# Kernel tuning notes

Hardware: AMD Instinct MI355X
Metric: run time of the kernel (lower is better)

Reference implementation:

```python
import jax, jax.numpy as jnp
import numpy as np

N_EMBD = 1024
HIDDEN = 4 * N_EMBD          # 4096
ADAPT = HIDDEN // 16         # 256
NUM_EXPERTS = 8
B, S = 4, 2048
LN_EPS = 1e-5


def setup_inputs() -> dict:
    key = jax.random.key(0)
    ks = jax.random.split(key, 8)
    x = jax.random.normal(ks[0], (B, S, N_EMBD), dtype=jnp.float32)
    # top-1 routing: one-hot expert weights (disjoint masks, standard MoE dispatch)
    route = jax.random.randint(ks[1], (B, S), 0, NUM_EXPERTS)
    expert_weights = jax.nn.one_hot(route, NUM_EXPERTS, dtype=jnp.float32)
    up_scale = 0.1 / N_EMBD ** 0.5
    adapt_scale0 = 0.1 / HIDDEN ** 0.5
    adapt_scale = 0.01 / ADAPT ** 0.5
    W_up = jax.random.normal(ks[2], (HIDDEN, N_EMBD), dtype=jnp.float32) * up_scale
    W_adapt = jax.random.normal(ks[3], (ADAPT, HIDDEN), dtype=jnp.float32) * adapt_scale0
    W_exp_adapters = jax.random.normal(ks[4], (NUM_EXPERTS, ADAPT, ADAPT), dtype=jnp.float32) * adapt_scale
    ln_gamma = jnp.ones((NUM_EXPERTS, ADAPT), dtype=jnp.float32)
    ln_beta = jnp.zeros((NUM_EXPERTS, ADAPT), dtype=jnp.float32)
    W_expert_proj = jax.random.normal(ks[5], (HIDDEN, ADAPT), dtype=jnp.float32) * adapt_scale
    W_out = jax.random.normal(ks[6], (N_EMBD, HIDDEN), dtype=jnp.float32) * adapt_scale
    return {"x": x, "expert_weights": expert_weights, "W_up": W_up,
            "W_adapt": W_adapt, "W_exp_adapters": W_exp_adapters,
            "ln_gamma": ln_gamma, "ln_beta": ln_beta,
            "W_expert_proj": W_expert_proj, "W_out": W_out}


def reference(x, expert_weights, W_up, W_adapt, W_exp_adapters, ln_gamma, ln_beta, W_expert_proj, W_out):
    b, s, d = x.shape
    T = b * s
    E = expert_weights.shape[-1]
    xt = x.reshape(T, d)

    # shared MLP path (silu(up_proj(x))) -> output_proj
    h = jax.nn.silu(xt @ W_up.T)                      # [T, HIDDEN]
    shared_out = (h @ W_out.T).reshape(b, s, d)       # [B, S, D]

    active = expert_weights.reshape(T, E) > 0         # [T, E]
    any_active = jnp.any(active, axis=-1)             # [T]
    last_idx = E - 1 - jnp.argmax(active[:, ::-1], axis=-1)  # [T]

    # pre_adapt (silu(up) recomputed == h) -> adapt_proj
    a = h @ W_adapt.T                                 # [T, ADAPT]
    # per-expert adapter linears, then select the winning expert per token
    a_all = jnp.einsum('td,eod->teo', a, W_exp_adapters)      # [T, E, ADAPT]
    a_sel = jnp.take_along_axis(a_all, last_idx[:, None, None], axis=1)[:, 0]  # [T, ADAPT]

    # per-expert LayerNorm params gathered per token
    g = ln_gamma[last_idx]                            # [T, ADAPT]
    be = ln_beta[last_idx]
    mu = jnp.mean(a_sel, axis=-1, keepdims=True)
    var = jnp.mean(jnp.square(a_sel - mu), axis=-1, keepdims=True)
    a_norm = (a_sel - mu) * jax.lax.rsqrt(var + LN_EPS) * g + be

    h2 = a_norm @ W_expert_proj.T                     # [T, HIDDEN]
    e_out = h2 @ W_out.T                              # [T, D]
    combined = jnp.where(any_active[:, None], e_out, 0.0).reshape(b, s, d)
    return shared_out + 0.1 * combined
```

## Files before the change

### kernel.cpp

```cpp
#include <hip/hip_runtime.h>
#include <cstdint>

#define TOK  8192
#define DEMB 1024
#define HID  4096
#define ADP  256
#define NEXP 8
#define KAUG 4352

typedef __bf16 bf16x8 __attribute__((ext_vector_type(8)));
typedef float  f32x4  __attribute__((ext_vector_type(4)));

__device__ __forceinline__ unsigned short f2bf(float f) {
  unsigned int u = __float_as_uint(f);
  u += 0x7fffu + ((u >> 16) & 1u);
  return (unsigned short)(u >> 16);
}
__device__ __forceinline__ float bf2f(unsigned short b) {
  return __uint_as_float(((unsigned int)b) << 16);
}

__global__ __launch_bounds__(256) void convert_all(
    const float* __restrict__ x, const float* __restrict__ wup,
    const float* __restrict__ wout, const float* __restrict__ wadapt,
    const float* __restrict__ wexp, const float* __restrict__ ew,
    const float* __restrict__ wp,
    unsigned short* __restrict__ xb, unsigned short* __restrict__ wub,
    unsigned short* __restrict__ wob, unsigned short* __restrict__ wab,
    unsigned short* __restrict__ web, int* __restrict__ route,
    unsigned short* __restrict__ wpT) {
  __shared__ float tile[64][65];
  int b = blockIdx.x;
  if (b >= 8992) {
    int wli = b - 8992;
    const int h0 = (wli & 63) * 64;
    const int a0 = (wli >> 6) * 64;
    const int t = threadIdx.x;
    const int r = t >> 4;
    const int c = (t & 15) * 4;
#pragma unroll
    for (int p = 0; p < 4; ++p) {
      int row = p * 16 + r;
      float4 v = *(const float4*)(wp + (size_t)(h0 + row) * ADP + a0 + c);
      tile[c + 0][row] = v.x;
      tile[c + 1][row] = v.y;
      tile[c + 2][row] = v.z;
      tile[c + 3][row] = v.w;
    }
    __syncthreads();
#pragma unroll
    for (int q = 0; q < 2; ++q) {
      int idx = q * 256 + t;
      int al = idx >> 3;
      int hg = (idx & 7) * 8;
      unsigned int w0 = (unsigned int)f2bf(tile[al][hg + 0]) |
                        ((unsigned int)f2bf(tile[al][hg + 1]) << 16);
      unsigned int w1 = (unsigned int)f2bf(tile[al][hg + 2]) |
                        ((unsigned int)f2bf(tile[al][hg + 3]) << 16);
      unsigned int w2 = (unsigned int)f2bf(tile[al][hg + 4]) |
                        ((unsigned int)f2bf(tile[al][hg + 5]) << 16);
      unsigned int w3 = (unsigned int)f2bf(tile[al][hg + 6]) |
                        ((unsigned int)f2bf(tile[al][hg + 7]) << 16);
      *(uint4*)(wpT + (size_t)(a0 + al) * HID + h0 + hg) =
          make_uint4(w0, w1, w2, w3);
    }
    return;
  }
  if (b >= 8960) {
    int t = (b - 8960) * 256 + threadIdx.x;
    const float* p = ew + (size_t)t * NEXP;
    int r = -1;
#pragma unroll
    for (int e = 0; e < NEXP; ++e)
      if (p[e] > 0.f) r = e;
    route[t] = r;
    return;
  }
  const float* src; unsigned short* dst; int lb; bool strided = false;
  if      (b < 4096) { src = x;      dst = xb;  lb = b; }
  else if (b < 6144) { src = wup;    dst = wub; lb = b - 4096; }
  else if (b < 8192) { src = wout;   dst = wob; lb = b - 6144; strided = true; }
  else if (b < 8704) { src = wadapt; dst = wab; lb = b - 8192; }
  else               { src = wexp;   dst = web; lb = b - 8704; }
  size_t base = (size_t)lb * 2048;
#pragma unroll
  for (int h = 0; h < 2; ++h) {
    size_t off = base + (size_t)h * 1024 + (size_t)threadIdx.x * 4;
    float4 v = *(const float4*)(src + off);
    ushort4 o;
    o.x = f2bf(v.x); o.y = f2bf(v.y); o.z = f2bf(v.z); o.w = f2bf(v.w);
    size_t doff = strided ? (off >> 12) * KAUG + (off & 4095) : off;
    *(ushort4*)(dst + doff) = o;
  }
}

__device__ __forceinline__ void remap_xcd(int li, int gx, int gy,
                                          int& bx, int& by) {
  int xcd = li & 7;
  int slot = li >> 3;
  bx = slot % gx;
  by = xcd * (gy >> 3) + slot / gx;
}

__device__ __forceinline__ void read_frag4(const unsigned short* base, int lane,
                                           int rowoff, int kk, bf16x8* dst) {
#pragma unroll
  for (int i = 0; i < 4; ++i) {
    int rr = rowoff + i * 16 + (lane & 15);
    int sw = ((kk >> 3) + (lane >> 4)) ^ (lane & 7);
    dst[i] = *(const bf16x8*)&base[rr * 64 + sw * 8];
  }
}

template <int NH>
__device__ __forceinline__ void mfma8(const bf16x8* af, const bf16x8* bf,
                                      f32x4 acc[4][4]) {
#pragma unroll
  for (int mt = 0; mt < 4; ++mt)
#pragma unroll
    for (int q = 0; q < 2; ++q)
      acc[mt][NH * 2 + q] = __builtin_amdgcn_mfma_f32_16x16x32_bf16(
          af[mt], bf[NH * 2 + q], acc[mt][NH * 2 + q], 0, 0, 0);
}

#define PHASE_MID()                                       \
  __builtin_amdgcn_s_barrier();                           \
  asm volatile("s_waitcnt lgkmcnt(0)" ::: "memory");      \
  __builtin_amdgcn_sched_barrier(0);                      \
  __builtin_amdgcn_s_setprio(1)

#define PHASE_END()                                       \
  __builtin_amdgcn_s_setprio(0);                          \
  __builtin_amdgcn_sched_barrier(0);                      \
  __builtin_amdgcn_s_barrier()

#define PHASE_END_VM(N)                                   \
  __builtin_amdgcn_s_setprio(0);                          \
  __builtin_amdgcn_sched_barrier(0);                      \
  asm volatile("s_waitcnt vmcnt(" #N ")" ::: "memory");   \
  __builtin_amdgcn_s_barrier()

template <int EPI>
__global__ __launch_bounds__(512, 2) void gemm8p(
    const unsigned short* __restrict__ A, int lda,
    const unsigned short* __restrict__ B, int ldb,
    void* __restrict__ C, int ldc, const int* __restrict__ route, int kLen) {
  __shared__ unsigned short As[2][128 * 64];
  __shared__ unsigned short Bs[2][256 * 64];
  const int lane = threadIdx.x & 63;
  const int wave = threadIdx.x >> 6;
  const int wm = wave >> 2, wn = wave & 3;
  int li = blockIdx.x + gridDim.x * blockIdx.y;
  int bx, by;
  remap_xcd(li, gridDim.x, gridDim.y, bx, by);
  const long rowBase = (long)by * 128;
  const long colBase = (long)bx * 256;
  const int srow = lane >> 3;
  const int scol = ((lane & 7) ^ (srow & 7)) * 8;
  const unsigned short* Ag = A + (rowBase + srow) * (long)lda + scol;
  const unsigned short* Bg = B + (colBase + srow) * (long)ldb + scol;
  const int NT = kLen >> 6;

  auto stA = [&](int buf, int t) {
#pragma unroll
    for (int c = 0; c < 2; ++c) {
      int chunk = wave * 2 + c;
      __builtin_amdgcn_global_load_lds(
          (const __attribute__((address_space(1))) unsigned int*)(uintptr_t)(
              Ag + (size_t)chunk * 8 * lda + (size_t)t * 64),
          (__attribute__((address_space(3))) unsigned int*)(uintptr_t)(
              &As[buf][chunk * 512]),
          16, 0, 0);
    }
  };
  auto stB = [&](int buf, int t, int h) {
#pragma unroll
    for (int c = 0; c < 2; ++c) {
      int chunk = h * 16 + wave * 2 + c;
      __builtin_amdgcn_global_load_lds(
          (const __attribute__((address_space(1))) unsigned int*)(uintptr_t)(
              Bg + (size_t)chunk * 8 * ldb + (size_t)t * 64),
          (__attribute__((address_space(3))) unsigned int*)(uintptr_t)(
              &Bs[buf][chunk * 512]),
          16, 0, 0);
    }
  };

  f32x4 acc[4][4] = {};
  bf16x8 af0[4], af1[4], bf0[4], bf1[4];

  stB(0, 0, 0);
  stB(0, 0, 1);
  stA(0, 0);
  if (NT > 1) {
    stA(1, 1);
    stB(1, 1, 0);
    asm volatile("s_waitcnt vmcnt(4)" ::: "memory");
  } else {
    asm volatile("s_waitcnt vmcnt(0)" ::: "memory");
  }
  __builtin_amdgcn_s_barrier();
  read_frag4(&As[0][0], lane, wm * 64, 0, af0);

  for (int t = 0; t < NT; ++t) {
    const int b = t & 1;
    read_frag4(&Bs[b][0], lane, wn * 64, 0, bf0);
    if (t + 1 < NT) stB(b ^ 1, t + 1, 1);
    PHASE_MID();
    mfma8<0>(af0, bf0, acc);
    PHASE_END();
    read_frag4(&As[b][0], lane, wm * 64, 32, af1);
    PHASE_MID();
    mfma8<1>(af0, bf0, acc);
    PHASE_END();
    read_frag4(&Bs[b][0], lane, wn * 64, 32, bf1);
    PHASE_MID();
    mfma8<0>(af1, bf1, acc);
    PHASE_END_VM(4);
    if (t + 1 < NT) read_frag4(&As[b ^ 1][0], lane, wm * 64, 0, af0);
    if (t + 2 < NT) { stA(b, t + 2); stB(b, t + 2, 0); }
    PHASE_MID();
    mfma8<1>(af1, bf1, acc);
    PHASE_END_VM(4);
  }

  const int rsub = (lane >> 4) * 4;
  const int csub = lane & 15;
#pragma unroll
  for (int mt = 0; mt < 4; ++mt) {
#pragma unroll
    for (int nt = 0; nt < 4; ++nt) {
      long col = colBase + wn * 64 + nt * 16 + csub;
#pragma unroll
      for (int r = 0; r < 4; ++r) {
        long row = rowBase + wm * 64 + mt * 16 + rsub + r;
        float v = acc[mt][nt][r];
        if (EPI == 0) {
          float s = __fdividef(v, 1.0f + __expf(-v));
          ((unsigned short*)C)[row * ldc + col] = f2bf(s);
        } else if (EPI == 1) {
          ((float*)C)[row * ldc + col] = v;
        } else {
          if (route[row] == (int)(col >> 8))
            ((float*)C)[row * ADP + (col & 255)] = v;
        }
      }
    }
  }
}

__device__ __forceinline__ void stage_tile(const unsigned short* __restrict__ g,
                                           int ldg, unsigned short* lds,
                                           int wave, int lane) {
  int srow = lane >> 3;
  int scol = ((lane & 7) ^ (srow & 7)) * 8;
#pragma unroll
  for (int c = 0; c < 4; ++c) {
    int chunk = wave * 4 + c;
    const unsigned short* gp = g + (size_t)(chunk * 8 + srow) * ldg + scol;
    unsigned short* lp = lds + chunk * 512;
    __builtin_amdgcn_global_load_lds(
        (const __attribute__((address_space(1))) unsigned int*)(uintptr_t)gp,
        (__attribute__((address_space(3))) unsigned int*)(uintptr_t)lp,
        16, 0, 0);
  }
}

__device__ __forceinline__ void gemm_body1(
    int bxr, int byr, int bz,
    const unsigned short* __restrict__ A, int lda,
    const unsigned short* __restrict__ B, int ldb,
    float* __restrict__ C, int ldc, int kLen, long splitStride,
    unsigned short* As, unsigned short* Bs) {
  const int lane = threadIdx.x & 63;
  const int wave = threadIdx.x >> 6;
  const int wm = wave >> 1, wn = wave & 1;
  const long rowBase = (long)byr * 128;
  const long colBase = (long)bxr * 128;
  const int ks = bz * kLen;
  const unsigned short* Ap = A + rowBase * lda + ks;
  const unsigned short* Bp = B + colBase * ldb + ks;
  f32x4 acc[4][4] = {};

  for (int kt = 0; kt < kLen; kt += 64) {
    stage_tile(Ap + kt, lda, As, wave, lane);
    stage_tile(Bp + kt, ldb, Bs, wave, lane);
    __syncthreads();
#pragma unroll
    for (int kk = 0; kk < 64; kk += 32) {
      const int kb = (kk >> 3) + (lane >> 4);
      const int sw = kb ^ (lane & 7);
      bf16x8 af[4], bfr[4];
#pragma unroll
      for (int mt = 0; mt < 4; ++mt) {
        int m = wm * 64 + mt * 16 + (lane & 15);
        af[mt] = *(const bf16x8*)&As[m * 64 + sw * 8];
      }
#pragma unroll
      for (int nt = 0; nt < 4; ++nt) {
        int n = wn * 64 + nt * 16 + (lane & 15);
        bfr[nt] = *(const bf16x8*)&Bs[n * 64 + sw * 8];
      }
#pragma unroll
      for (int mt = 0; mt < 4; ++mt)
#pragma unroll
        for (int nt = 0; nt < 4; ++nt)
          acc[mt][nt] = __builtin_amdgcn_mfma_f32_16x16x32_bf16(
              af[mt], bfr[nt], acc[mt][nt], 0, 0, 0);
    }
    __syncthreads();
  }

  const int rsub = (lane >> 4) * 4;
  const int csub = lane & 15;
#pragma unroll
  for (int mt = 0; mt < 4; ++mt) {
#pragma unroll
    for (int nt = 0; nt < 4; ++nt) {
      long col = colBase + wn * 64 + nt * 16 + csub;
#pragma unroll
      for (int r = 0; r < 4; ++r) {
        long row = rowBase + wm * 64 + mt * 16 + rsub + r;
        (C + splitStride * bz)[row * ldc + col] = acc[mt][nt][r];
      }
    }
  }
}

__global__ __launch_bounds__(256, 3) void gemm_dual(
    const unsigned short* __restrict__ A0, int lda0,
    const unsigned short* __restrict__ B0, int ldb0,
    float* __restrict__ C0, int ldc0, int kLen0, long ss0, int gx0, int gy0,
    int nb0,
    const unsigned short* __restrict__ A1, int lda1,
    const unsigned short* __restrict__ B1, int ldb1,
    float* __restrict__ C1, int ldc1, int kLen1, long ss1, int gx1, int gy1) {
  __shared__ unsigned short As[128 * 64];
  __shared__ unsigned short Bs[128 * 64];
  int li = blockIdx.x;
  if (li < nb0) {
    int per = gx0 * gy0;
    int z = li / per, rem = li % per;
    int bx, by;
    remap_xcd(rem, gx0, gy0, bx, by);
    gemm_body1(bx, by, z, A0, lda0, B0, ldb0, C0, ldc0, kLen0, ss0, As, Bs);
  } else {
    int wli = li - nb0;
    int per = gx1 * gy1;
    int z = wli / per, rem = wli % per;
    int bx, by;
    remap_xcd(rem, gx1, gy1, bx, by);
    gemm_body1(bx, by, z, A1, lda1, B1, ldb1, C1, ldc1, kLen1, ss1, As, Bs);
  }
}

__global__ __launch_bounds__(256) void reduce_both(
    const float* __restrict__ P, unsigned short* __restrict__ ab,
    const float* __restrict__ Pw, unsigned short* __restrict__ wob) {
  int b = blockIdx.x;
  if (b < 2048) {
    size_t i = ((size_t)b * 256 + threadIdx.x) * 4;
    const size_t stride = (size_t)TOK * ADP;
    float4 p0 = *(const float4*)(P + i);
    float4 p1 = *(const float4*)(P + stride + i);
    float4 p2 = *(const float4*)(P + 2 * stride + i);
    float4 p3 = *(const float4*)(P + 3 * stride + i);
    ushort4 o;
    o.x = f2bf(p0.x + p1.x + p2.x + p3.x);
    o.y = f2bf(p0.y + p1.y + p2.y + p3.y);
    o.z = f2bf(p0.z + p1.z + p2.z + p3.z);
    o.w = f2bf(p0.w + p1.w + p2.w + p3.w);
    *(ushort4*)(ab + i) = o;
  } else {
    size_t i = ((size_t)(b - 2048) * 256 + threadIdx.x) * 4;
    const size_t stride = (size_t)DEMB * ADP;
    float4 s = *(const float4*)(Pw + i);
#pragma unroll
    for (int k = 1; k < 8; ++k) {
      float4 p = *(const float4*)(Pw + k * stride + i);
      s.x += p.x; s.y += p.y; s.z += p.z; s.w += p.w;
    }
    size_t d = i >> 8, a = i & 255;
    ushort4 o;
    o.x = f2bf(0.1f * s.x); o.y = f2bf(0.1f * s.y);
    o.z = f2bf(0.1f * s.z); o.w = f2bf(0.1f * s.w);
    *(ushort4*)(wob + d * KAUG + HID + a) = o;
  }
}

__global__ __launch_bounds__(256) void ln_kernel(
    const float* __restrict__ asel, const int* __restrict__ route,
    const float* __restrict__ gamma, const float* __restrict__ beta,
    unsigned short* __restrict__ haug) {
  const int lane = threadIdx.x & 63;
  const int t = blockIdx.x * 4 + (threadIdx.x >> 6);
  const int e = route[t];
  float4 v = *(const float4*)(asel + (size_t)t * ADP + lane * 4);
  float s1 = v.x + v.y + v.z + v.w;
  float s2 = v.x * v.x + v.y * v.y + v.z * v.z + v.w * v.w;
#pragma unroll
  for (int off = 32; off > 0; off >>= 1) {
    s1 += __shfl_down(s1, off);
    s2 += __shfl_down(s2, off);
  }
  s1 = __shfl(s1, 0);
  s2 = __shfl(s2, 0);
  float mu = s1 * (1.0f / ADP);
  float var = s2 * (1.0f / ADP) - mu * mu;
  float rstd = rsqrtf(var + 1e-5f);
  ushort4 o;
  if (e >= 0) {
    float4 g = *(const float4*)(gamma + (size_t)e * ADP + lane * 4);
    float4 b = *(const float4*)(beta + (size_t)e * ADP + lane * 4);
    o.x = f2bf((v.x - mu) * rstd * g.x + b.x);
    o.y = f2bf((v.y - mu) * rstd * g.y + b.y);
    o.z = f2bf((v.z - mu) * rstd * g.z + b.z);
    o.w = f2bf((v.w - mu) * rstd * g.w + b.w);
  } else {
    o.x = o.y = o.z = o.w = 0;
  }
  *(ushort4*)(haug + (size_t)t * KAUG + HID + lane * 4) = o;
}

extern "C" void kernel_launch(void* const* d_in, const int* in_sizes, int n_in,
                              void* d_out, int out_size, void* d_ws, size_t ws_size,
                              hipStream_t stream) {
  const float* x     = (const float*)d_in[0];
  const float* ew    = (const float*)d_in[1];
  const float* W_up  = (const float*)d_in[2];
  const float* W_ad  = (const float*)d_in[3];
  const float* W_ex  = (const float*)d_in[4];
  const float* gam   = (const float*)d_in[5];
  const float* bet   = (const float*)d_in[6];
  const float* W_pr  = (const float*)d_in[7];
  const float* W_out = (const float*)d_in[8];
  float* out = (float*)d_out;

  char* ws = (char*)d_ws;
  size_t off = 0;
  auto alloc = [&](size_t n) {
    char* p = ws + off;
    off += (n + 255) & ~(size_t)255;
    return p;
  };
  unsigned short* xb   = (unsigned short*)alloc((size_t)TOK * DEMB * 2);
  unsigned short* wub  = (unsigned short*)alloc((size_t)HID * DEMB * 2);
  unsigned short* wob  = (unsigned short*)alloc((size_t)DEMB * KAUG * 2);
  unsigned short* wab  = (unsigned short*)alloc((size_t)ADP * HID * 2);
  unsigned short* web  = (unsigned short*)alloc((size_t)NEXP * ADP * ADP * 2);
  unsigned short* wpT  = (unsigned short*)alloc((size_t)ADP * HID * 2);
  unsigned short* Haug = (unsigned short*)alloc((size_t)TOK * KAUG * 2);
  float*          P    = (float*)alloc((size_t)4 * TOK * ADP * 4);
  float*          Pw   = (float*)alloc((size_t)8 * DEMB * ADP * 4);
  unsigned short* ab   = (unsigned short*)alloc((size_t)TOK * ADP * 2);
  int*          route  = (int*)alloc((size_t)TOK * 4);
  float* asel = P;

  convert_all<<<9248, 256, 0, stream>>>(x, W_up, W_out, W_ad, W_ex, ew, W_pr,
                                        xb, wub, wob, wab, web, route, wpT);
  gemm8p<0><<<dim3(HID / 256, TOK / 128, 1), 512, 0, stream>>>(
      xb, DEMB, wub, DEMB, Haug, KAUG, nullptr, DEMB);
  gemm_dual<<<640, 256, 0, stream>>>(
      Haug, KAUG, wab, HID, P, ADP, HID / 4, (long)TOK * ADP, 2, 64, 512,
      wob, KAUG, wpT, HID, Pw, ADP, HID / 8, (long)DEMB * ADP, 2, 8);
  reduce_both<<<2304, 256, 0, stream>>>(P, ab, Pw, wob);
  gemm8p<3><<<dim3(NEXP * ADP / 256, TOK / 128, 1), 512, 0, stream>>>(
      ab, ADP, web, ADP, asel, ADP, route, ADP);
  ln_kernel<<<TOK / 4, 256, 0, stream>>>(asel, route, gam, bet, Haug);
  gemm8p<1><<<dim3(DEMB / 256, TOK / 128, 1), 512, 0, stream>>>(
      Haug, KAUG, wob, KAUG, out, DEMB, nullptr, KAUG);
}
```

Before: 359.3 us.

## Add 256x256 tiled GEMM kernel for up-projection and expert-adapter GEMMs

Introduces a new gemm256 kernel that uses 256x256 output tiles with 8 waves, each computing a 128x64 sub-tile arranged as four quadrant phases. Ping-pong register fragments and global-to-LDS loads are interleaved with the MFMA phases. It replaces the 128x256 gemm8p for the up-projection and the expert-adapter GEMMs. The larger tile raises arithmetic intensity and operand reuse per LDS load, but it doubles LDS use and accumulator registers, which could limit occupancy, and it halves the number of blocks.

```diff
diff --git a/kernel.cpp b/kernel.cpp
--- a/kernel.cpp
+++ b/kernel.cpp
@@ -102,27 +102,6 @@
   by = xcd * (gy >> 3) + slot / gx;
 }
 
-__device__ __forceinline__ void read_frag4(const unsigned short* base, int lane,
-                                           int rowoff, int kk, bf16x8* dst) {
-#pragma unroll
-  for (int i = 0; i < 4; ++i) {
-    int rr = rowoff + i * 16 + (lane & 15);
-    int sw = ((kk >> 3) + (lane >> 4)) ^ (lane & 7);
-    dst[i] = *(const bf16x8*)&base[rr * 64 + sw * 8];
-  }
-}
-
-template <int NH>
-__device__ __forceinline__ void mfma8(const bf16x8* af, const bf16x8* bf,
-                                      f32x4 acc[4][4]) {
-#pragma unroll
-  for (int mt = 0; mt < 4; ++mt)
-#pragma unroll
-    for (int q = 0; q < 2; ++q)
-      acc[mt][NH * 2 + q] = __builtin_amdgcn_mfma_f32_16x16x32_bf16(
-          af[mt], bf[NH * 2 + q], acc[mt][NH * 2 + q], 0, 0, 0);
-}
-
 #define PHASE_MID()                                       \
   __builtin_amdgcn_s_barrier();                           \
   asm volatile("s_waitcnt lgkmcnt(0)" ::: "memory");      \
@@ -139,6 +118,156 @@
   __builtin_amdgcn_sched_barrier(0);                      \
   asm volatile("s_waitcnt vmcnt(" #N ")" ::: "memory");   \
   __builtin_amdgcn_s_barrier()
+
+template <int MB, int NB>
+__device__ __forceinline__ void mfmaQ(const bf16x8 af[4][2], const bf16x8 bf[2][2],
+                                      f32x4 acc[8][4]) {
+#pragma unroll
+  for (int mt = 0; mt < 4; ++mt)
+#pragma unroll
+    for (int nt = 0; nt < 2; ++nt)
+#pragma unroll
+      for (int kk = 0; kk < 2; ++kk)
+        acc[MB + mt][NB + nt] = __builtin_amdgcn_mfma_f32_16x16x32_bf16(
+            af[mt][kk], bf[nt][kk], acc[MB + mt][NB + nt], 0, 0, 0);
+}
+
+template <int EPI>
+__global__ __launch_bounds__(512, 2) void gemm256(
+    const unsigned short* __restrict__ A, int lda,
+    const unsigned short* __restrict__ B, int ldb,
+    void* __restrict__ C, int ldc, const int* __restrict__ route, int kLen) {
+  __shared__ unsigned short As[2][256 * 64];
+  __shared__ unsigned short Bs[2][256 * 64];
+  const int lane = threadIdx.x & 63;
+  const int wave = threadIdx.x >> 6;
+  const int wm = wave >> 2, wn = wave & 3;
+  int li = blockIdx.x + gridDim.x * blockIdx.y;
+  int bx, by;
+  remap_xcd(li, gridDim.x, gridDim.y, bx, by);
+  const long rowBase = (long)by * 256;
+  const long colBase = (long)bx * 256;
+  const int srow = lane >> 3;
+  const int scol = ((lane & 7) ^ (srow & 7)) * 8;
+  const unsigned short* Ag = A + (rowBase + srow) * (long)lda + scol;
+  const unsigned short* Bg = B + (colBase + srow) * (long)ldb + scol;
+  const int NT = kLen >> 6;
+
+  auto st2 = [&](unsigned short* lds, const unsigned short* g, long ld, int t,
+                 int half) {
+#pragma unroll
+    for (int c = 0; c < 2; ++c) {
+      int chunk = half * 16 + wave * 2 + c;
+      __builtin_amdgcn_global_load_lds(
+          (const __attribute__((address_space(1))) unsigned int*)(uintptr_t)(
+              g + (size_t)chunk * 8 * ld + (size_t)t * 64),
+          (__attribute__((address_space(3))) unsigned int*)(uintptr_t)(
+              lds + chunk * 512),
+          16, 0, 0);
+    }
+  };
+  auto rdA = [&](const unsigned short* base, int mhalf, bf16x8 dst[4][2]) {
+#pragma unroll
+    for (int mt = 0; mt < 4; ++mt)
+#pragma unroll
+      for (int kk = 0; kk < 2; ++kk) {
+        int rr = mhalf * 128 + wm * 64 + mt * 16 + (lane & 15);
+        int sw = (kk * 4 + (lane >> 4)) ^ (lane & 7);
+        dst[mt][kk] = *(const bf16x8*)&base[rr * 64 + sw * 8];
+      }
+  };
+  auto rdB = [&](const unsigned short* base, int nhalf, bf16x8 dst[2][2]) {
+#pragma unroll
+    for (int nt = 0; nt < 2; ++nt)
+#pragma unroll
+      for (int kk = 0; kk < 2; ++kk) {
+        int rr = nhalf * 128 + wn * 32 + nt * 16 + (lane & 15);
+        int sw = (kk * 4 + (lane >> 4)) ^ (lane & 7);
+        dst[nt][kk] = *(const bf16x8*)&base[rr * 64 + sw * 8];
+      }
+  };
+
+  f32x4 acc[8][4] = {};
+  bf16x8 afA[4][2], afB[4][2], bfA[2][2], bfB[2][2];
+
+  st2(As[0], Ag, lda, 0, 0);
+  st2(Bs[0], Bg, ldb, 0, 0);
+  st2(Bs[0], Bg, ldb, 0, 1);
+  st2(As[0], Ag, lda, 0, 1);
+  asm volatile("s_waitcnt vmcnt(0)" ::: "memory");
+  __builtin_amdgcn_s_barrier();
+  rdA(As[0], 0, afA);
+  rdB(Bs[0], 0, bfA);
+
+  for (int t = 0; t < NT; ++t) {
+    const int b = t & 1;
+    unsigned short* Asn = As[b ^ 1];
+    unsigned short* Bsn = Bs[b ^ 1];
+    rdB(Bs[b], 1, bfB);
+    if (t + 1 < NT) { st2(Asn, Ag, lda, t + 1, 0); st2(Bsn, Bg, ldb, t + 1, 0); }
+    PHASE_MID();
+    mfmaQ<0, 0>(afA, bfA, acc);
+    PHASE_END_VM(4);
+    rdA(As[b], 1, afB);
+    if (t + 1 < NT) { st2(Bsn, Bg, ldb, t + 1, 1); st2(Asn, Ag, lda, t + 1, 1); }
+    PHASE_MID();
+    mfmaQ<0, 2>(afA, bfB, acc);
+    PHASE_END_VM(6);
+    if (t + 1 < NT) rdA(Asn, 0, afA);
+    PHASE_MID();
+    mfmaQ<4, 0>(afB, bfA, acc);
+    PHASE_END_VM(4);
+    if (t + 1 < NT) rdB(Bsn, 0, bfA);
+    PHASE_MID();
+    mfmaQ<4, 2>(afB, bfB, acc);
+    if (t + 2 < NT) { PHASE_END_VM(2); } else { PHASE_END_VM(0); }
+  }
+
+  const int rsub = (lane >> 4) * 4;
+  const int csub = lane & 15;
+#pragma unroll
+  for (int mt = 0; mt < 8; ++mt) {
+#pragma unroll
+    for (int nt = 0; nt < 4; ++nt) {
+      long col = colBase + (nt >> 1) * 128 + wn * 32 + (nt & 1) * 16 + csub;
+#pragma unroll
+      for (int r = 0; r < 4; ++r) {
+        long row = rowBase + (mt >> 2) * 128 + wm * 64 + (mt & 3) * 16 + rsub + r;
+        float v = acc[mt][nt][r];
+        if (EPI == 0) {
+          float s = __fdividef(v, 1.0f + __expf(-v));
+          ((unsigned short*)C)[row * ldc + col] = f2bf(s);
+        } else if (EPI == 1) {
+          ((float*)C)[row * ldc + col] = v;
+        } else {
+          if (route[row] == (int)(col >> 8))
+            ((float*)C)[row * ADP + (col & 255)] = v;
+        }
+      }
+    }
+  }
+}
+
+__device__ __forceinline__ void read_frag4(const unsigned short* base, int lane,
+                                           int rowoff, int kk, bf16x8* dst) {
+#pragma unroll
+  for (int i = 0; i < 4; ++i) {
+    int rr = rowoff + i * 16 + (lane & 15);
+    int sw = ((kk >> 3) + (lane >> 4)) ^ (lane & 7);
+    dst[i] = *(const bf16x8*)&base[rr * 64 + sw * 8];
+  }
+}
+
+template <int NH>
+__device__ __forceinline__ void mfma8(const bf16x8* af, const bf16x8* bf,
+                                      f32x4 acc[4][4]) {
+#pragma unroll
+  for (int mt = 0; mt < 4; ++mt)
+#pragma unroll
+    for (int q = 0; q < 2; ++q)
+      acc[mt][NH * 2 + q] = __builtin_amdgcn_mfma_f32_16x16x32_bf16(
+          af[mt], bf[NH * 2 + q], acc[mt][NH * 2 + q], 0, 0, 0);
+}
 
 template <int EPI>
 __global__ __launch_bounds__(512, 2) void gemm8p(
@@ -458,13 +587,13 @@
 
   convert_all<<<9248, 256, 0, stream>>>(x, W_up, W_out, W_ad, W_ex, ew, W_pr,
                                         xb, wub, wob, wab, web, route, wpT);
-  gemm8p<0><<<dim3(HID / 256, TOK / 128, 1), 512, 0, stream>>>(
+  gemm256<0><<<dim3(HID / 256, TOK / 256, 1), 512, 0, stream>>>(
       xb, DEMB, wub, DEMB, Haug, KAUG, nullptr, DEMB);
   gemm_dual<<<640, 256, 0, stream>>>(
       Haug, KAUG, wab, HID, P, ADP, HID / 4, (long)TOK * ADP, 2, 64, 512,
       wob, KAUG, wpT, HID, Pw, ADP, HID / 8, (long)DEMB * ADP, 2, 8);
   reduce_both<<<2304, 256, 0, stream>>>(P, ab, Pw, wob);
-  gemm8p<3><<<dim3(NEXP * ADP / 256, TOK / 128, 1), 512, 0, stream>>>(
+  gemm256<3><<<dim3(NEXP * ADP / 256, TOK / 256, 1), 512, 0, stream>>>(
       ab, ADP, web, ADP, asel, ADP, route, ADP);
   ln_kernel<<<TOK / 4, 256, 0, stream>>>(asel, route, gam, bet, Haug);
   gemm8p<1><<<dim3(DEMB / 256, TOK / 128, 1), 512, 0, stream>>>(
```

After: 348.7 us. 1.03x faster.

## Fuse weight conversion with up-proj GEMM and fuse LayerNorm into expert GEMM

Applied to the files above, without the earlier changes.

Splits the conversion pass so only x and W_up are converted first. The remaining weight conversions and the transpose of W_expert_proj then run as extra blocks of a combined kernel alongside the up-projection GEMM. The up-projection now uses the simpler single-buffered 128x128 GEMM body instead of the pipelined 128x256 kernel. The expert adapter GEMM computes per-row mean and variance in its epilogue and writes the normalized bf16 values directly, removing the fp32 intermediate and the separate LN launch. The risk is a slower main GEMM, because it loses the double-buffered pipeline.

```diff
diff --git a/kernel.cpp b/kernel.cpp
--- a/kernel.cpp
+++ b/kernel.cpp
@@ -20,54 +20,14 @@
   return __uint_as_float(((unsigned int)b) << 16);
 }
 
-__global__ __launch_bounds__(256) void convert_all(
+__global__ __launch_bounds__(256) void convert_a(
     const float* __restrict__ x, const float* __restrict__ wup,
-    const float* __restrict__ wout, const float* __restrict__ wadapt,
-    const float* __restrict__ wexp, const float* __restrict__ ew,
-    const float* __restrict__ wp,
+    const float* __restrict__ ew,
     unsigned short* __restrict__ xb, unsigned short* __restrict__ wub,
-    unsigned short* __restrict__ wob, unsigned short* __restrict__ wab,
-    unsigned short* __restrict__ web, int* __restrict__ route,
-    unsigned short* __restrict__ wpT) {
-  __shared__ float tile[64][65];
+    int* __restrict__ route) {
   int b = blockIdx.x;
-  if (b >= 8992) {
-    int wli = b - 8992;
-    const int h0 = (wli & 63) * 64;
-    const int a0 = (wli >> 6) * 64;
-    const int t = threadIdx.x;
-    const int r = t >> 4;
-    const int c = (t & 15) * 4;
-#pragma unroll
-    for (int p = 0; p < 4; ++p) {
-      int row = p * 16 + r;
-      float4 v = *(const float4*)(wp + (size_t)(h0 + row) * ADP + a0 + c);
-      tile[c + 0][row] = v.x;
-      tile[c + 1][row] = v.y;
-      tile[c + 2][row] = v.z;
-      tile[c + 3][row] = v.w;
-    }
-    __syncthreads();
-#pragma unroll
-    for (int q = 0; q < 2; ++q) {
-      int idx = q * 256 + t;
-      int al = idx >> 3;
-      int hg = (idx & 7) * 8;
-      unsigned int w0 = (unsigned int)f2bf(tile[al][hg + 0]) |
-                        ((unsigned int)f2bf(tile[al][hg + 1]) << 16);
-      unsigned int w1 = (unsigned int)f2bf(tile[al][hg + 2]) |
-                        ((unsigned int)f2bf(tile[al][hg + 3]) << 16);
-      unsigned int w2 = (unsigned int)f2bf(tile[al][hg + 4]) |
-                        ((unsigned int)f2bf(tile[al][hg + 5]) << 16);
-      unsigned int w3 = (unsigned int)f2bf(tile[al][hg + 6]) |
-                        ((unsigned int)f2bf(tile[al][hg + 7]) << 16);
-      *(uint4*)(wpT + (size_t)(a0 + al) * HID + h0 + hg) =
-          make_uint4(w0, w1, w2, w3);
-    }
-    return;
-  }
-  if (b >= 8960) {
-    int t = (b - 8960) * 256 + threadIdx.x;
+  if (b >= 6144) {
+    int t = (b - 6144) * 256 + threadIdx.x;
     const float* p = ew + (size_t)t * NEXP;
     int r = -1;
 #pragma unroll
@@ -76,12 +36,9 @@
     route[t] = r;
     return;
   }
-  const float* src; unsigned short* dst; int lb; bool strided = false;
-  if      (b < 4096) { src = x;      dst = xb;  lb = b; }
-  else if (b < 6144) { src = wup;    dst = wub; lb = b - 4096; }
-  else if (b < 8192) { src = wout;   dst = wob; lb = b - 6144; strided = true; }
-  else if (b < 8704) { src = wadapt; dst = wab; lb = b - 8192; }
-  else               { src = wexp;   dst = web; lb = b - 8704; }
+  const float* src; unsigned short* dst; int lb;
+  if (b < 4096) { src = x;   dst = xb;  lb = b; }
+  else          { src = wup; dst = wub; lb = b - 4096; }
   size_t base = (size_t)lb * 2048;
 #pragma unroll
   for (int h = 0; h < 2; ++h) {
@@ -89,8 +46,7 @@
     float4 v = *(const float4*)(src + off);
     ushort4 o;
     o.x = f2bf(v.x); o.y = f2bf(v.y); o.z = f2bf(v.z); o.w = f2bf(v.w);
-    size_t doff = strided ? (off >> 12) * KAUG + (off & 4095) : off;
-    *(ushort4*)(dst + doff) = o;
+    *(ushort4*)(dst + off) = o;
   }
 }
 
@@ -102,27 +58,6 @@
   by = xcd * (gy >> 3) + slot / gx;
 }
 
-__device__ __forceinline__ void read_frag4(const unsigned short* base, int lane,
-                                           int rowoff, int kk, bf16x8* dst) {
-#pragma unroll
-  for (int i = 0; i < 4; ++i) {
-    int rr = rowoff + i * 16 + (lane & 15);
-    int sw = ((kk >> 3) + (lane >> 4)) ^ (lane & 7);
-    dst[i] = *(const bf16x8*)&base[rr * 64 + sw * 8];
-  }
-}
-
-template <int NH>
-__device__ __forceinline__ void mfma8(const bf16x8* af, const bf16x8* bf,
-                                      f32x4 acc[4][4]) {
-#pragma unroll
-  for (int mt = 0; mt < 4; ++mt)
-#pragma unroll
-    for (int q = 0; q < 2; ++q)
-      acc[mt][NH * 2 + q] = __builtin_amdgcn_mfma_f32_16x16x32_bf16(
-          af[mt], bf[NH * 2 + q], acc[mt][NH * 2 + q], 0, 0, 0);
-}
-
 #define PHASE_MID()                                       \
   __builtin_amdgcn_s_barrier();                           \
   asm volatile("s_waitcnt lgkmcnt(0)" ::: "memory");      \
@@ -140,11 +75,212 @@
   asm volatile("s_waitcnt vmcnt(" #N ")" ::: "memory");   \
   __builtin_amdgcn_s_barrier()
 
+__device__ __forceinline__ void stage_tile(const unsigned short* __restrict__ g,
+                                           int ldg, unsigned short* lds,
+                                           int wave, int lane) {
+  int srow = lane >> 3;
+  int scol = ((lane & 7) ^ (srow & 7)) * 8;
+#pragma unroll
+  for (int c = 0; c < 4; ++c) {
+    int chunk = wave * 4 + c;
+    const unsigned short* gp = g + (size_t)(chunk * 8 + srow) * ldg + scol;
+    unsigned short* lp = lds + chunk * 512;
+    __builtin_amdgcn_global_load_lds(
+        (const __attribute__((address_space(1))) unsigned int*)(uintptr_t)gp,
+        (__attribute__((address_space(3))) unsigned int*)(uintptr_t)lp,
+        16, 0, 0);
+  }
+}
+
 template <int EPI>
+__device__ __forceinline__ void gemm_body(
+    int bxr, int byr, int bz,
+    const unsigned short* __restrict__ A, int lda,
+    const unsigned short* __restrict__ B, int ldb,
+    void* __restrict__ C, int ldc, int kLen, long splitStride,
+    unsigned short* As, unsigned short* Bs) {
+  const int lane = threadIdx.x & 63;
+  const int wave = threadIdx.x >> 6;
+  const int wm = wave >> 1, wn = wave & 1;
+  const long rowBase = (long)byr * 128;
+  const long colBase = (long)bxr * 128;
+  const int ks = bz * kLen;
+  const unsigned short* Ap = A + rowBase * lda + ks;
+  const unsigned short* Bp = B + colBase * ldb + ks;
+  f32x4 acc[4][4] = {};
+
+  for (int kt = 0; kt < kLen; kt += 64) {
+    stage_tile(Ap + kt, lda, As, wave, lane);
+    stage_tile(Bp + kt, ldb, Bs, wave, lane);
+    __syncthreads();
+#pragma unroll
+    for (int kk = 0; kk < 64; kk += 32) {
+      const int kb = (kk >> 3) + (lane >> 4);
+      const int sw = kb ^ (lane & 7);
+      bf16x8 af[4], bfr[4];
+#pragma unroll
+      for (int mt = 0; mt < 4; ++mt) {
+        int m = wm * 64 + mt * 16 + (lane & 15);
+        af[mt] = *(const bf16x8*)&As[m * 64 + sw * 8];
+      }
+#pragma unroll
+      for (int nt = 0; nt < 4; ++nt) {
+        int n = wn * 64 + nt * 16 + (lane & 15);
+        bfr[nt] = *(const bf16x8*)&Bs[n * 64 + sw * 8];
+      }
+#pragma unroll
+      for (int mt = 0; mt < 4; ++mt)
+#pragma unroll
+        for (int nt = 0; nt < 4; ++nt)
+          acc[mt][nt] = __builtin_amdgcn_mfma_f32_16x16x32_bf16(
+              af[mt], bfr[nt], acc[mt][nt], 0, 0, 0);
+    }
+    __syncthreads();
+  }
+
+  const int rsub = (lane >> 4) * 4;
+  const int csub = lane & 15;
+#pragma unroll
+  for (int mt = 0; mt < 4; ++mt) {
+#pragma unroll
+    for (int nt = 0; nt < 4; ++nt) {
+      long col = colBase + wn * 64 + nt * 16 + csub;
+#pragma unroll
+      for (int r = 0; r < 4; ++r) {
+        long row = rowBase + wm * 64 + mt * 16 + rsub + r;
+        float v = acc[mt][nt][r];
+        if (EPI == 0) {
+          float s = __fdividef(v, 1.0f + __expf(-v));
+          ((unsigned short*)C)[row * ldc + col] = f2bf(s);
+        } else {
+          ((float*)C + splitStride * bz)[row * ldc + col] = v;
+        }
+      }
+    }
+  }
+}
+
+__global__ __launch_bounds__(256, 3) void fused2(
+    const unsigned short* __restrict__ xb, const unsigned short* __restrict__ wub,
+    unsigned short* __restrict__ haug,
+    const float* __restrict__ wout, const float* __restrict__ wadapt,
+    const float* __restrict__ wexp, const float* __restrict__ wp,
+    unsigned short* __restrict__ wob, unsigned short* __restrict__ wab,
+    unsigned short* __restrict__ web, unsigned short* __restrict__ wpT) {
+  __shared__ char smem[32768];
+  int li = blockIdx.x;
+  if (li < 2048) {
+    int bx, by;
+    remap_xcd(li, 32, 64, bx, by);
+    gemm_body<0>(bx, by, 0, xb, DEMB, wub, DEMB, haug, KAUG, DEMB, 0,
+                 (unsigned short*)smem, (unsigned short*)(smem + 16384));
+    return;
+  }
+  int cb = li - 2048;
+  if (cb < 2816) {
+    const float* src; unsigned short* dst; int lb; bool strided = false;
+    if (cb < 2048)      { src = wout;   dst = wob; lb = cb;        strided = true; }
+    else if (cb < 2560) { src = wadapt; dst = wab; lb = cb - 2048; }
+    else                { src = wexp;   dst = web; lb = cb - 2560; }
+    size_t base = (size_t)lb * 2048;
+#pragma unroll
+    for (int h = 0; h < 2; ++h) {
+      size_t off = base + (size_t)h * 1024 + (size_t)threadIdx.x * 4;
+      float4 v = *(const float4*)(src + off);
+      ushort4 o;
+      o.x = f2bf(v.x); o.y = f2bf(v.y); o.z = f2bf(v.z); o.w = f2bf(v.w);
+      size_t doff = strided ? (off >> 12) * KAUG + (off & 4095) : off;
+      *(ushort4*)(dst + doff) = o;
+    }
+    return;
+  }
+  float (*tile)[65] = (float(*)[65])smem;
+  int wli = cb - 2816;
+  const int h0 = (wli & 63) * 64;
+  const int a0 = (wli >> 6) * 64;
+  const int t = threadIdx.x;
+  const int r = t >> 4;
+  const int c = (t & 15) * 4;
+#pragma unroll
+  for (int p = 0; p < 4; ++p) {
+    int row = p * 16 + r;
+    float4 v = *(const float4*)(wp + (size_t)(h0 + row) * ADP + a0 + c);
+    tile[c + 0][row] = v.x;
+    tile[c + 1][row] = v.y;
+    tile[c + 2][row] = v.z;
+    tile[c + 3][row] = v.w;
+  }
+  __syncthreads();
+#pragma unroll
+  for (int q = 0; q < 2; ++q) {
+    int idx = q * 256 + t;
+    int al = idx >> 3;
+    int hg = (idx & 7) * 8;
+    unsigned int w0 = (unsigned int)f2bf(tile[al][hg + 0]) |
+                      ((unsigned int)f2bf(tile[al][hg + 1]) << 16);
+    unsigned int w1 = (unsigned int)f2bf(tile[al][hg + 2]) |
+                      ((unsigned int)f2bf(tile[al][hg + 3]) << 16);
+    unsigned int w2 = (unsigned int)f2bf(tile[al][hg + 4]) |
+                      ((unsigned int)f2bf(tile[al][hg + 5]) << 16);
+    unsigned int w3 = (unsigned int)f2bf(tile[al][hg + 6]) |
+                      ((unsigned int)f2bf(tile[al][hg + 7]) << 16);
+    *(uint4*)(wpT + (size_t)(a0 + al) * HID + h0 + hg) =
+        make_uint4(w0, w1, w2, w3);
+  }
+}
+
+__global__ __launch_bounds__(256, 3) void gemm_dual(
+    const unsigned short* __restrict__ A0, int lda0,
+    const unsigned short* __restrict__ B0, int ldb0,
+    float* __restrict__ C0, int ldc0, int kLen0, long ss0, int gx0, int gy0,
+    int nb0,
+    const unsigned short* __restrict__ A1, int lda1,
+    const unsigned short* __restrict__ B1, int ldb1,
+    float* __restrict__ C1, int ldc1, int kLen1, long ss1, int gx1, int gy1) {
+  __shared__ unsigned short As[128 * 64];
+  __shared__ unsigned short Bs[128 * 64];
+  int li = blockIdx.x;
+  if (li < nb0) {
+    int per = gx0 * gy0;
+    int z = li / per, rem = li % per;
+    int bx, by;
+    remap_xcd(rem, gx0, gy0, bx, by);
+    gemm_body<1>(bx, by, z, A0, lda0, B0, ldb0, C0, ldc0, kLen0, ss0, As, Bs);
+  } else {
+    int wli = li - nb0;
+    int per = gx1 * gy1;
+    int z = wli / per, rem = wli % per;
+    int bx, by;
+    remap_xcd(rem, gx1, gy1, bx, by);
+    gemm_body<1>(bx, by, z, A1, lda1, B1, ldb1, C1, ldc1, kLen1, ss1, As, Bs);
+  }
+}
+
+__device__ __forceinline__ void read_frag4(const unsigned short* base, int lane,
+                                           int rowoff, int kk, bf16x8* dst) {
+#pragma unroll
+  for (int i = 0; i < 4; ++i) {
+    int rr = rowoff + i * 16 + (lane & 15);
+    int sw = ((kk >> 3) + (lane >> 4)) ^ (lane & 7);
+    dst[i] = *(const bf16x8*)&base[rr * 64 + sw * 8];
+  }
+}
+
+template <int NH>
+__device__ __forceinline__ void mfma8(const bf16x8* af, const bf16x8* bf,
+                                      f32x4 acc[4][4]) {
+#pragma unroll
+  for (int mt = 0; mt < 4; ++mt)
+#pragma unroll
+    for (int q = 0; q < 2; ++q)
+      acc[mt][NH * 2 + q] = __builtin_amdgcn_mfma_f32_16x16x32_bf16(
+          af[mt], bf[NH * 2 + q], acc[mt][NH * 2 + q], 0, 0, 0);
+}
+
 __global__ __launch_bounds__(512, 2) void gemm8p(
     const unsigned short* __restrict__ A, int lda,
     const unsigned short* __restrict__ B, int ldb,
-    void* __restrict__ C, int ldc, const int* __restrict__ route, int kLen) {
+    float* __restrict__ C, int ldc, int kLen) {
   __shared__ unsigned short As[2][128 * 64];
   __shared__ unsigned short Bs[2][256 * 64];
   const int lane = threadIdx.x & 63;
@@ -234,123 +370,9 @@
 #pragma unroll
       for (int r = 0; r < 4; ++r) {
         long row = rowBase + wm * 64 + mt * 16 + rsub + r;
-        float v = acc[mt][nt][r];
-        if (EPI == 0) {
-          float s = __fdividef(v, 1.0f + __expf(-v));
-          ((unsigned short*)C)[row * ldc + col] = f2bf(s);
-        } else if (EPI == 1) {
-          ((float*)C)[row * ldc + col] = v;
-        } else {
-          if (route[row] == (int)(col >> 8))
-            ((float*)C)[row * ADP + (col & 255)] = v;
-        }
-      }
-    }
-  }
-}
-
-__device__ __forceinline__ void stage_tile(const unsigned short* __restrict__ g,
-                                           int ldg, unsigned short* lds,
-                                           int wave, int lane) {
-  int srow = lane >> 3;
-  int scol = ((lane & 7) ^ (srow & 7)) * 8;
-#pragma unroll
-  for (int c = 0; c < 4; ++c) {
-    int chunk = wave * 4 + c;
-    const unsigned short* gp = g + (size_t)(chunk * 8 + srow) * ldg + scol;
-    unsigned short* lp = lds + chunk * 512;
-    __builtin_amdgcn_global_load_lds(
-        (const __attribute__((address_space(1))) unsigned int*)(uintptr_t)gp,
-        (__attribute__((address_space(3))) unsigned int*)(uintptr_t)lp,
-        16, 0, 0);
-  }
-}
-
-__device__ __forceinline__ void gemm_body1(
-    int bxr, int byr, int bz,
-    const unsigned short* __restrict__ A, int lda,
-    const unsigned short* __restrict__ B, int ldb,
-    float* __restrict__ C, int ldc, int kLen, long splitStride,
-    unsigned short* As, unsigned short* Bs) {
-  const int lane = threadIdx.x & 63;
-  const int wave = threadIdx.x >> 6;
-  const int wm = wave >> 1, wn = wave & 1;
-  const long rowBase = (long)byr * 128;
-  const long colBase = (long)bxr * 128;
-  const int ks = bz * kLen;
-  const unsigned short* Ap = A + rowBase * lda + ks;
-  const unsigned short* Bp = B + colBase * ldb + ks;
-  f32x4 acc[4][4] = {};
-
-  for (int kt = 0; kt < kLen; kt += 64) {
-    stage_tile(Ap + kt, lda, As, wave, lane);
-    stage_tile(Bp + kt, ldb, Bs, wave, lane);
-    __syncthreads();
-#pragma unroll
-    for (int kk = 0; kk < 64; kk += 32) {
-      const int kb = (kk >> 3) + (lane >> 4);
-      const int sw = kb ^ (lane & 7);
-      bf16x8 af[4], bfr[4];
-#pragma unroll
-      for (int mt = 0; mt < 4; ++mt) {
-        int m = wm * 64 + mt * 16 + (lane & 15);
-        af[mt] = *(const bf16x8*)&As[m * 64 + sw * 8];
-      }
-#pragma unroll
-      for (int nt = 0; nt < 4; ++nt) {
-        int n = wn * 64 + nt * 16 + (lane & 15);
-        bfr[nt] = *(const bf16x8*)&Bs[n * 64 + sw * 8];
-      }
-#pragma unroll
-      for (int mt = 0; mt < 4; ++mt)
-#pragma unroll
-        for (int nt = 0; nt < 4; ++nt)
-          acc[mt][nt] = __builtin_amdgcn_mfma_f32_16x16x32_bf16(
-              af[mt], bfr[nt], acc[mt][nt], 0, 0, 0);
-    }
-    __syncthreads();
-  }
-
-  const int rsub = (lane >> 4) * 4;
-  const int csub = lane & 15;
-#pragma unroll
-  for (int mt = 0; mt < 4; ++mt) {
-#pragma unroll
-    for (int nt = 0; nt < 4; ++nt) {
-      long col = colBase + wn * 64 + nt * 16 + csub;
-#pragma unroll
-      for (int r = 0; r < 4; ++r) {
-        long row = rowBase + wm * 64 + mt * 16 + rsub + r;
-        (C + splitStride * bz)[row * ldc + col] = acc[mt][nt][r];
-      }
-    }
-  }
-}
-
-__global__ __launch_bounds__(256, 3) void gemm_dual(
-    const unsigned short* __restrict__ A0, int lda0,
-    const unsigned short* __restrict__ B0, int ldb0,
-    float* __restrict__ C0, int ldc0, int kLen0, long ss0, int gx0, int gy0,
-    int nb0,
-    const unsigned short* __restrict__ A1, int lda1,
-    const unsigned short* __restrict__ B1, int ldb1,
-    float* __restrict__ C1, int ldc1, int kLen1, long ss1, int gx1, int gy1) {
-  __shared__ unsigned short As[128 * 64];
-  __shared__ unsigned short Bs[128 * 64];
-  int li = blockIdx.x;
-  if (li < nb0) {
-    int per = gx0 * gy0;
-    int z = li / per, rem = li % per;
-    int bx, by;
-    remap_xcd(rem, gx0, gy0, bx, by);
-    gemm_body1(bx, by, z, A0, lda0, B0, ldb0, C0, ldc0, kLen0, ss0, As, Bs);
-  } else {
-    int wli = li - nb0;
-    int per = gx1 * gy1;
-    int z = wli / per, rem = wli % per;
-    int bx, by;
-    remap_xcd(rem, gx1, gy1, bx, by);
-    gemm_body1(bx, by, z, A1, lda1, B1, ldb1, C1, ldc1, kLen1, ss1, As, Bs);
+        C[row * ldc + col] = acc[mt][nt][r];
+      }
+    }
   }
 }
 
@@ -388,38 +410,139 @@
   }
 }
 
-__global__ __launch_bounds__(256) void ln_kernel(
-    const float* __restrict__ asel, const int* __restrict__ route,
+__global__ __launch_bounds__(512, 2) void gemm_exp_ln(
+    const unsigned short* __restrict__ A,
+    const unsigned short* __restrict__ Wexp,
+    const int* __restrict__ route,
     const float* __restrict__ gamma, const float* __restrict__ beta,
     unsigned short* __restrict__ haug) {
+  __shared__ unsigned short As[128 * 64];
+  __shared__ unsigned short Bs[256 * 64];
+  __shared__ float red1[4][128];
+  __shared__ float red2[4][128];
   const int lane = threadIdx.x & 63;
-  const int t = blockIdx.x * 4 + (threadIdx.x >> 6);
-  const int e = route[t];
-  float4 v = *(const float4*)(asel + (size_t)t * ADP + lane * 4);
-  float s1 = v.x + v.y + v.z + v.w;
-  float s2 = v.x * v.x + v.y * v.y + v.z * v.z + v.w * v.w;
-#pragma unroll
-  for (int off = 32; off > 0; off >>= 1) {
-    s1 += __shfl_down(s1, off);
-    s2 += __shfl_down(s2, off);
-  }
-  s1 = __shfl(s1, 0);
-  s2 = __shfl(s2, 0);
-  float mu = s1 * (1.0f / ADP);
-  float var = s2 * (1.0f / ADP) - mu * mu;
-  float rstd = rsqrtf(var + 1e-5f);
-  ushort4 o;
-  if (e >= 0) {
-    float4 g = *(const float4*)(gamma + (size_t)e * ADP + lane * 4);
-    float4 b = *(const float4*)(beta + (size_t)e * ADP + lane * 4);
-    o.x = f2bf((v.x - mu) * rstd * g.x + b.x);
-    o.y = f2bf((v.y - mu) * rstd * g.y + b.y);
-    o.z = f2bf((v.z - mu) * rstd * g.z + b.z);
-    o.w = f2bf((v.w - mu) * rstd * g.w + b.w);
-  } else {
-    o.x = o.y = o.z = o.w = 0;
-  }
-  *(ushort4*)(haug + (size_t)t * KAUG + HID + lane * 4) = o;
+  const int wave = threadIdx.x >> 6;
+  const int wm = wave >> 2, wn = wave & 3;
+  int li = blockIdx.x + gridDim.x * blockIdx.y;
+  int bx, by;
+  remap_xcd(li, gridDim.x, gridDim.y, bx, by);
+  const long rowBase = (long)by * 128;
+  const unsigned short* Ap = A + rowBase * ADP;
+  const unsigned short* Bp = Wexp + (size_t)bx * ADP * ADP;
+  const int srow = lane >> 3;
+  const int scol = ((lane & 7) ^ (srow & 7)) * 8;
+  f32x4 acc[4][4] = {};
+
+  for (int kt = 0; kt < ADP; kt += 64) {
+#pragma unroll
+    for (int c = 0; c < 2; ++c) {
+      int chunk = wave * 2 + c;
+      __builtin_amdgcn_global_load_lds(
+          (const __attribute__((address_space(1))) unsigned int*)(uintptr_t)(
+              Ap + (size_t)(chunk * 8 + srow) * ADP + kt + scol),
+          (__attribute__((address_space(3))) unsigned int*)(uintptr_t)(
+              As + chunk * 512),
+          16, 0, 0);
+    }
+#pragma unroll
+    for (int c = 0; c < 4; ++c) {
+      int chunk = wave * 4 + c;
+      __builtin_amdgcn_global_load_lds(
+          (const __attribute__((address_space(1))) unsigned int*)(uintptr_t)(
+              Bp + (size_t)(chunk * 8 + srow) * ADP + kt + scol),
+          (__attribute__((address_space(3))) unsigned int*)(uintptr_t)(
+              Bs + chunk * 512),
+          16, 0, 0);
+    }
+    __syncthreads();
+#pragma unroll
+    for (int kk = 0; kk < 64; kk += 32) {
+      const int kb = (kk >> 3) + (lane >> 4);
+      const int sw = kb ^ (lane & 7);
+      bf16x8 af[4], bfr[4];
+#pragma unroll
+      for (int mt = 0; mt < 4; ++mt) {
+        int m = wm * 64 + mt * 16 + (lane & 15);
+        af[mt] = *(const bf16x8*)&As[m * 64 + sw * 8];
+      }
+#pragma unroll
+      for (int nt = 0; nt < 4; ++nt) {
+        int n = wn * 64 + nt * 16 + (lane & 15);
+        bfr[nt] = *(const bf16x8*)&Bs[n * 64 + sw * 8];
+      }
+#pragma unroll
+      for (int mt = 0; mt < 4; ++mt)
+#pragma unroll
+        for (int nt = 0; nt < 4; ++nt)
+          acc[mt][nt] = __builtin_amdgcn_mfma_f32_16x16x32_bf16(
+              af[mt], bfr[nt], acc[mt][nt], 0, 0, 0);
+    }
+    __syncthreads();
+  }
+
+  float ls1[4][4], ls2[4][4];
+#pragma unroll
+  for (int mt = 0; mt < 4; ++mt)
+#pragma unroll
+    for (int r = 0; r < 4; ++r) {
+      float s1 = 0.f, s2 = 0.f;
+#pragma unroll
+      for (int nt = 0; nt < 4; ++nt) {
+        float v = acc[mt][nt][r];
+        s1 += v; s2 += v * v;
+      }
+      ls1[mt][r] = s1; ls2[mt][r] = s2;
+    }
+#pragma unroll
+  for (int m = 1; m < 16; m <<= 1)
+#pragma unroll
+    for (int mt = 0; mt < 4; ++mt)
+#pragma unroll
+      for (int r = 0; r < 4; ++r) {
+        ls1[mt][r] += __shfl_xor(ls1[mt][r], m);
+        ls2[mt][r] += __shfl_xor(ls2[mt][r], m);
+      }
+  if ((lane & 15) == 0) {
+    int g = lane >> 4;
+#pragma unroll
+    for (int mt = 0; mt < 4; ++mt)
+#pragma unroll
+      for (int r = 0; r < 4; ++r) {
+        int rl = wm * 64 + mt * 16 + g * 4 + r;
+        red1[wn][rl] = ls1[mt][r];
+        red2[wn][rl] = ls2[mt][r];
+      }
+  }
+  __syncthreads();
+  const int rsub = (lane >> 4) * 4;
+  const int csub = lane & 15;
+  float gv[4], bv[4];
+#pragma unroll
+  for (int nt = 0; nt < 4; ++nt) {
+    int col = wn * 64 + nt * 16 + csub;
+    gv[nt] = gamma[bx * ADP + col];
+    bv[nt] = beta[bx * ADP + col];
+  }
+#pragma unroll
+  for (int mt = 0; mt < 4; ++mt) {
+#pragma unroll
+    for (int r = 0; r < 4; ++r) {
+      int rl = wm * 64 + mt * 16 + rsub + r;
+      long row = rowBase + rl;
+      if (route[row] != bx) continue;
+      float t1 = red1[0][rl] + red1[1][rl] + red1[2][rl] + red1[3][rl];
+      float t2 = red2[0][rl] + red2[1][rl] + red2[2][rl] + red2[3][rl];
+      float mu = t1 * (1.0f / ADP);
+      float var = t2 * (1.0f / ADP) - mu * mu;
+      float rstd = rsqrtf(var + 1e-5f);
+#pragma unroll
+      for (int nt = 0; nt < 4; ++nt) {
+        int col = wn * 64 + nt * 16 + csub;
+        float val = (acc[mt][nt][r] - mu) * rstd * gv[nt] + bv[nt];
+        haug[row * KAUG + HID + col] = f2bf(val);
+      }
+    }
+  }
 }
 
 extern "C" void kernel_launch(void* const* d_in, const int* in_sizes, int n_in,
@@ -454,19 +577,16 @@
   float*          Pw   = (float*)alloc((size_t)8 * DEMB * ADP * 4);
   unsigned short* ab   = (unsigned short*)alloc((size_t)TOK * ADP * 2);
   int*          route  = (int*)alloc((size_t)TOK * 4);
-  float* asel = P;
-
-  convert_all<<<9248, 256, 0, stream>>>(x, W_up, W_out, W_ad, W_ex, ew, W_pr,
-                                        xb, wub, wob, wab, web, route, wpT);
-  gemm8p<0><<<dim3(HID / 256, TOK / 128, 1), 512, 0, stream>>>(
-      xb, DEMB, wub, DEMB, Haug, KAUG, nullptr, DEMB);
+
+  convert_a<<<6176, 256, 0, stream>>>(x, W_up, ew, xb, wub, route);
+  fused2<<<5120, 256, 0, stream>>>(xb, wub, Haug, W_out, W_ad, W_ex, W_pr,
+                                   wob, wab, web, wpT);
   gemm_dual<<<640, 256, 0, stream>>>(
       Haug, KAUG, wab, HID, P, ADP, HID / 4, (long)TOK * ADP, 2, 64, 512,
       wob, KAUG, wpT, HID, Pw, ADP, HID / 8, (long)DEMB * ADP, 2, 8);
   reduce_both<<<2304, 256, 0, stream>>>(P, ab, Pw, wob);
-  gemm8p<3><<<dim3(NEXP * ADP / 256, TOK / 128, 1), 512, 0, stream>>>(
-      ab, ADP, web, ADP, asel, ADP, route, ADP);
-  ln_kernel<<<TOK / 4, 256, 0, stream>>>(asel, route, gam, bet, Haug);
-  gemm8p<1><<<dim3(DEMB / 256, TOK / 128, 1), 512, 0, stream>>>(
-      Haug, KAUG, wob, KAUG, out, DEMB, nullptr, KAUG);
-}
+  gemm_exp_ln<<<dim3(NEXP, TOK / 128), 512, 0, stream>>>(
+      ab, web, route, gam, bet, Haug);
+  gemm8p<<<dim3(DEMB / 256, TOK / 128), 512, 0, stream>>>(
+      Haug, KAUG, wob, KAUG, out, DEMB, KAUG);
+}
```

Measured after the change: 336.9 us. -6.2%, faster.
